# Kernel tuning notes

Hardware: AMD Instinct MI355X
Metric: run time of the kernel (lower is better)

Reference implementation:

```python
import jax, jax.numpy as jnp
import numpy as np


def _gcn_conv(x, edge_index, edge_weight, W, b, n_nodes):
    # PyG GCNConv with normalize=True: add self-loops (weight 1), symmetric norm,
    # transform then aggregate: out[col] += norm * (x @ W)[row], plus bias.
    row = jnp.concatenate([edge_index[0], jnp.arange(n_nodes)])
    col = jnp.concatenate([edge_index[1], jnp.arange(n_nodes)])
    w = jnp.concatenate([edge_weight, jnp.ones((n_nodes,), x.dtype)])
    deg = jax.ops.segment_sum(w, col, num_segments=n_nodes)
    dinv = jnp.where(deg > 0, jax.lax.rsqrt(jnp.maximum(deg, 1e-12)), 0.0)
    norm = dinv[row] * w * dinv[col]            # [E+N]
    h = x @ W                                   # [N, out]
    msg = h[row] * norm[:, None]                # [E+N, out]
    out = jax.ops.segment_sum(msg, col, num_segments=n_nodes)
    return out + b


def setup_inputs() -> dict:
    key = jax.random.key(0)
    ks = jax.random.split(key, 6)
    N, E, F_IN, H, C = 50000, 800000, 512, 128, 40
    features = jax.random.normal(ks[0], (N, F_IN), jnp.float32)
    edge_index = jax.random.randint(ks[1], (2, E), 0, N, jnp.int64)
    edge_weight = jax.random.uniform(ks[2], (E,), jnp.float32)
    W1 = jax.random.normal(ks[3], (F_IN, H), jnp.float32) * 0.05
    b1 = jnp.zeros((H,), jnp.float32)
    W2 = jax.random.normal(ks[4], (H, C), jnp.float32) * 0.05
    b2 = jnp.zeros((C,), jnp.float32)
    return {"features": features, "edge_index": edge_index, "edge_weight": edge_weight,
            "W1": W1, "b1": b1, "W2": W2, "b2": b2}


def reference(features, edge_index, edge_weight, W1, b1, W2, b2):
    n_nodes = features.shape[0]
    x = _gcn_conv(features, edge_index, edge_weight, W1, b1, n_nodes)
    x = jax.nn.relu(x)
    # F.dropout(training=self.training): identity in eval mode
    x = _gcn_conv(x, edge_index, edge_weight, W2, b2, n_nodes)
    return jax.nn.log_softmax(x, axis=1)
```

## Files before the change

kernel.cpp:

```cpp
#include <hip/hip_runtime.h>
#include <math.h>

#define FIN  512
#define HDIM 128
#define CDIM 40
#define CPAD 48
#define CAP  64

typedef __attribute__((ext_vector_type(8))) short shortx8;
typedef __attribute__((ext_vector_type(4))) float f32x4;
typedef __attribute__((ext_vector_type(2))) float floatx2;

__device__ inline unsigned short f2bf(float x) {
    unsigned u = __builtin_bit_cast(unsigned, x);
    unsigned r = u + 0x7fffu + ((u >> 16) & 1u);
    return (unsigned short)(r >> 16);
}
__device__ inline float bfu(unsigned short v) { return __builtin_bit_cast(float, (unsigned)v << 16); }
__device__ inline float bflo(unsigned u) { return __builtin_bit_cast(float, u << 16); }
__device__ inline float bfhi(unsigned u) { return __builtin_bit_cast(float, u & 0xffff0000u); }
__device__ inline float wdec(unsigned p) { return __builtin_bit_cast(float, (p & 0x7fffu) << 16); }
__device__ inline unsigned char f2fp8(float x) {
    return (unsigned char)(__builtin_amdgcn_cvt_pk_fp8_f32(x, x, 0, false) & 0xff);
}
__device__ inline floatx2 fp8x2_dec(unsigned short v) {
    return __builtin_amdgcn_cvt_pk_f32_fp8((int)(unsigned)v, false);
}

__global__ void k_fill(const int* __restrict__ row, const int* __restrict__ col,
                       const float* __restrict__ w,
                       unsigned long long* __restrict__ cursor,
                       unsigned* __restrict__ bkt, int E) {
    int e = blockIdx.x * blockDim.x + threadIdx.x;
    if (e >= E) return;
    const int c = col[e];
    const float we = w[e];
    const unsigned long long wfix = (unsigned long long)(we * 4294967296.0f);
    const unsigned long long old = atomicAdd(&cursor[c], (1ULL << 40) | wfix);
    const int p = (int)(old >> 40);
    const unsigned wb = (__builtin_bit_cast(unsigned, we) + 0x8000u) >> 16;
    if (p < CAP) bkt[(size_t)c * CAP + p] = ((unsigned)row[e] << 15) | (wb & 0x7fffu);
}

#define PREPB 280
__global__ void k_prep(const float* __restrict__ W1, const float* __restrict__ W2,
                       unsigned short* __restrict__ W1T, unsigned short* __restrict__ W2T,
                       const unsigned long long* __restrict__ cursor,
                       int* __restrict__ cnt, float* __restrict__ dinv, int n) {
    const int b = blockIdx.x;
    if (b < PREPB) {
        const int i = b * 256 + threadIdx.x;
        if (i < FIN * HDIM) {
            const int k = i >> 7, nn = i & 127;
            W1T[nn * FIN + k] = f2bf(W1[i]);
        } else {
            const int j = i - FIN * HDIM;
            const int nn = j >> 7, k = j & 127;
            W2T[j] = (nn < CDIM) ? f2bf(W2[k * CDIM + nn]) : (unsigned short)0;
        }
    } else {
        const int i = (b - PREPB) * 256 + threadIdx.x;
        if (i < n) {
            const unsigned long long p = cursor[i];
            cnt[i] = min((int)(p >> 40), CAP);
            const float wsum = (float)(p & ((1ULL << 40) - 1)) * 2.3283064365386963e-10f;
            dinv[i] = rsqrtf(1.0f + wsum);
        }
    }
}

#define G1_LDA 72
__global__ __launch_bounds__(256) void k_gemm1(const float* __restrict__ A,
                                               const unsigned short* __restrict__ W1T,
                                               const float* __restrict__ dinv,
                                               unsigned char* __restrict__ h1f8, int M) {
    __shared__ short As[128 * G1_LDA];
    __shared__ short Bs[128 * G1_LDA];
    const int tid  = threadIdx.x;
    const int wave = tid >> 6;
    const int lane = tid & 63;
    const int quad = lane >> 4;
    const int mr   = lane & 15;
    const int m0w  = (wave & 1) * 64;
    const int n0w  = (wave >> 1) * 64;
    const int m0b  = blockIdx.x * 128;

    const int srow = tid >> 1;
    const int spart = tid & 1;

    f32x4 acc[4][4];
#pragma unroll
    for (int i = 0; i < 4; i++)
#pragma unroll
        for (int j = 0; j < 4; j++) acc[i][j] = (f32x4)0.f;

    const int grow = m0b + srow;
    const bool arow_ok = grow < M;
    const float* ap = A + (size_t)grow * FIN + spart * 32;
    const unsigned short* bp = W1T + (size_t)srow * FIN + spart * 32;

    for (int k0 = 0; k0 < FIN; k0 += 64) {
#pragma unroll
        for (int i = 0; i < 4; i++) {
            float4 v0 = make_float4(0.f, 0.f, 0.f, 0.f), v1 = v0;
            if (arow_ok) {
                v0 = *(const float4*)(ap + k0 + i * 8);
                v1 = *(const float4*)(ap + k0 + i * 8 + 4);
            }
            shortx8 pk;
            pk[0] = (short)f2bf(v0.x); pk[1] = (short)f2bf(v0.y);
            pk[2] = (short)f2bf(v0.z); pk[3] = (short)f2bf(v0.w);
            pk[4] = (short)f2bf(v1.x); pk[5] = (short)f2bf(v1.y);
            pk[6] = (short)f2bf(v1.z); pk[7] = (short)f2bf(v1.w);
            *(shortx8*)&As[srow * G1_LDA + spart * 32 + i * 8] = pk;
        }
#pragma unroll
        for (int i = 0; i < 4; i++)
            *(shortx8*)&Bs[srow * G1_LDA + spart * 32 + i * 8] =
                *(const shortx8*)(bp + k0 + i * 8);
        __syncthreads();

#pragma unroll
        for (int kk = 0; kk < 2; kk++) {
            shortx8 af[4], bfr[4];
#pragma unroll
            for (int mt = 0; mt < 4; mt++)
                af[mt] = *(shortx8*)&As[(m0w + mt * 16 + mr) * G1_LDA + kk * 32 + quad * 8];
#pragma unroll
            for (int nt = 0; nt < 4; nt++)
                bfr[nt] = *(shortx8*)&Bs[(n0w + nt * 16 + mr) * G1_LDA + kk * 32 + quad * 8];
#pragma unroll
            for (int mt = 0; mt < 4; mt++)
#pragma unroll
                for (int nt = 0; nt < 4; nt++)
                    acc[mt][nt] = __builtin_amdgcn_mfma_f32_16x16x32_bf16(
                        af[mt], bfr[nt], acc[mt][nt], 0, 0, 0);
        }
        __syncthreads();
    }
#pragma unroll
    for (int mt = 0; mt < 4; mt++)
#pragma unroll
        for (int r = 0; r < 4; r++) {
            const int om = m0b + m0w + mt * 16 + quad * 4 + r;
            if (om < M) {
                const float dv = dinv[om];
#pragma unroll
                for (int nt = 0; nt < 4; nt++)
                    h1f8[(size_t)om * HDIM + n0w + nt * 16 + mr] = f2fp8(dv * acc[mt][nt][r]);
            }
        }
}

__global__ __launch_bounds__(256) void k_gather1(
    const int* __restrict__ cnt_arr, const unsigned* __restrict__ bkt,
    const unsigned char* __restrict__ h1f8,
    const float* __restrict__ dinv, const float* __restrict__ b1,
    unsigned* __restrict__ x1u, int n_nodes) {
    const int node = blockIdx.x * 4 + (threadIdx.x >> 6);
    const int lane = threadIdx.x & 63;
    if (node >= n_nodes) return;
    const int cnt = cnt_arr[node];
    const unsigned* base = bkt + (size_t)node * CAP;
    const int loff = lane * 2;
    float a0 = 0.f, a1 = 0.f, c0 = 0.f, c1 = 0.f;
    int s = 0;
    for (; s + 8 <= cnt; s += 8) {
        const uint4 qa = *(const uint4*)(base + s);
        const uint4 qb = *(const uint4*)(base + s + 4);
        const unsigned short v0 = *(const unsigned short*)(h1f8 + (size_t)(qa.x >> 15) * HDIM + loff);
        const unsigned short v1 = *(const unsigned short*)(h1f8 + (size_t)(qa.y >> 15) * HDIM + loff);
        const unsigned short v2 = *(const unsigned short*)(h1f8 + (size_t)(qa.z >> 15) * HDIM + loff);
        const unsigned short v3 = *(const unsigned short*)(h1f8 + (size_t)(qa.w >> 15) * HDIM + loff);
        const unsigned short v4 = *(const unsigned short*)(h1f8 + (size_t)(qb.x >> 15) * HDIM + loff);
        const unsigned short v5 = *(const unsigned short*)(h1f8 + (size_t)(qb.y >> 15) * HDIM + loff);
        const unsigned short v6 = *(const unsigned short*)(h1f8 + (size_t)(qb.z >> 15) * HDIM + loff);
        const unsigned short v7 = *(const unsigned short*)(h1f8 + (size_t)(qb.w >> 15) * HDIM + loff);
        const floatx2 f0 = fp8x2_dec(v0), f1 = fp8x2_dec(v1), f2 = fp8x2_dec(v2), f3 = fp8x2_dec(v3);
        const floatx2 f4 = fp8x2_dec(v4), f5 = fp8x2_dec(v5), f6 = fp8x2_dec(v6), f7 = fp8x2_dec(v7);
        a0 += wdec(qa.x) * f0.x + wdec(qa.y) * f1.x + wdec(qa.z) * f2.x + wdec(qa.w) * f3.x;
        a1 += wdec(qa.x) * f0.y + wdec(qa.y) * f1.y + wdec(qa.z) * f2.y + wdec(qa.w) * f3.y;
        c0 += wdec(qb.x) * f4.x + wdec(qb.y) * f5.x + wdec(qb.z) * f6.x + wdec(qb.w) * f7.x;
        c1 += wdec(qb.x) * f4.y + wdec(qb.y) * f5.y + wdec(qb.z) * f6.y + wdec(qb.w) * f7.y;
    }
    for (; s + 4 <= cnt; s += 4) {
        const uint4 qa = *(const uint4*)(base + s);
        const unsigned short v0 = *(const unsigned short*)(h1f8 + (size_t)(qa.x >> 15) * HDIM + loff);
        const unsigned short v1 = *(const unsigned short*)(h1f8 + (size_t)(qa.y >> 15) * HDIM + loff);
        const unsigned short v2 = *(const unsigned short*)(h1f8 + (size_t)(qa.z >> 15) * HDIM + loff);
        const unsigned short v3 = *(const unsigned short*)(h1f8 + (size_t)(qa.w >> 15) * HDIM + loff);
        const floatx2 f0 = fp8x2_dec(v0), f1 = fp8x2_dec(v1), f2 = fp8x2_dec(v2), f3 = fp8x2_dec(v3);
        a0 += wdec(qa.x) * f0.x + wdec(qa.y) * f1.x + wdec(qa.z) * f2.x + wdec(qa.w) * f3.x;
        a1 += wdec(qa.x) * f0.y + wdec(qa.y) * f1.y + wdec(qa.z) * f2.y + wdec(qa.w) * f3.y;
    }
    for (; s < cnt; s++) {
        const unsigned p = base[s];
        const unsigned short v = *(const unsigned short*)(h1f8 + (size_t)(p >> 15) * HDIM + loff);
        const floatx2 f = fp8x2_dec(v);
        a0 += wdec(p) * f.x;
        a1 += wdec(p) * f.y;
    }
    a0 += c0; a1 += c1;
    const float dl = dinv[node];
    const unsigned short vs = *(const unsigned short*)(h1f8 + (size_t)node * HDIM + loff);
    const floatx2 fs = fp8x2_dec(vs);
    a0 = fmaxf(dl * (a0 + fs.x) + b1[loff], 0.f);
    a1 = fmaxf(dl * (a1 + fs.y) + b1[loff + 1], 0.f);
    x1u[(size_t)node * 64 + lane] = (unsigned)f2bf(a0) | ((unsigned)f2bf(a1) << 16);
}

#define G2_LDA 136
__global__ __launch_bounds__(256) void k_gemm2(const unsigned short* __restrict__ x1bf,
                                               const unsigned short* __restrict__ W2T,
                                               const float* __restrict__ dinv,
                                               unsigned short* __restrict__ h2a,
                                               unsigned short* __restrict__ h2b, int M) {
    __shared__ short Xs[128 * G2_LDA];
    __shared__ short Ws[CPAD * G2_LDA];
    const int tid  = threadIdx.x;
    const int wave = tid >> 6;
    const int lane = tid & 63;
    const int quad = lane >> 4;
    const int mr   = lane & 15;
    const int m0b  = blockIdx.x * 128;

    {
        const int srow = tid >> 1, spart = tid & 1;
        const int grow = m0b + srow;
        if (grow < M) {
            const unsigned short* xp = x1bf + (size_t)grow * HDIM + spart * 64;
#pragma unroll
            for (int i = 0; i < 8; i++)
                *(shortx8*)&Xs[srow * G2_LDA + spart * 64 + i * 8] = *(const shortx8*)(xp + i * 8);
        } else {
#pragma unroll
            for (int i = 0; i < 8; i++)
                *(shortx8*)&Xs[srow * G2_LDA + spart * 64 + i * 8] = (shortx8)0;
        }
        for (int idx = tid; idx < CPAD * 16; idx += 256) {
            const int r = idx >> 4, j = idx & 15;
            *(shortx8*)&Ws[r * G2_LDA + j * 8] = *(const shortx8*)(W2T + r * HDIM + j * 8);
        }
    }
    __syncthreads();

    f32x4 acc[2][3];
#pragma unroll
    for (int i = 0; i < 2; i++)
#pragma unroll
        for (int j = 0; j < 3; j++) acc[i][j] = (f32x4)0.f;

    const int m0w = wave * 32;
#pragma unroll
    for (int kk = 0; kk < 4; kk++) {
        shortx8 af[2], bfr[3];
#pragma unroll
        for (int mt = 0; mt < 2; mt++)
            af[mt] = *(shortx8*)&Xs[(m0w + mt * 16 + mr) * G2_LDA + kk * 32 + quad * 8];
#pragma unroll
        for (int nt = 0; nt < 3; nt++)
            bfr[nt] = *(shortx8*)&Ws[(nt * 16 + mr) * G2_LDA + kk * 32 + quad * 8];
#pragma unroll
        for (int mt = 0; mt < 2; mt++)
#pragma unroll
            for (int nt = 0; nt < 3; nt++)
                acc[mt][nt] = __builtin_amdgcn_mfma_f32_16x16x32_bf16(
                    af[mt], bfr[nt], acc[mt][nt], 0, 0, 0);
    }
#pragma unroll
    for (int mt = 0; mt < 2; mt++)
#pragma unroll
        for (int r = 0; r < 4; r++) {
            const int om = m0b + m0w + mt * 16 + quad * 4 + r;
            if (om < M) {
                const float dv = dinv[om];
#pragma unroll
                for (int nt = 0; nt < 2; nt++)
                    h2a[(size_t)om * 32 + nt * 16 + mr] = f2bf(dv * acc[mt][nt][r]);
                if (mr < 8)
                    h2b[(size_t)om * 8 + mr] = f2bf(dv * acc[mt][2][r]);
            }
        }
}

__global__ __launch_bounds__(256) void k_gather2(
    const int* __restrict__ cnt_arr, const unsigned* __restrict__ bkt,
    const unsigned short* __restrict__ h2a, const unsigned short* __restrict__ h2b,
    const float* __restrict__ dinv, const float* __restrict__ b2,
    float* __restrict__ out, int n_nodes) {
    const int node = blockIdx.x * 4 + (threadIdx.x >> 6);
    const int lane = threadIdx.x & 63;
    if (node >= n_nodes) return;
    const bool act = lane < CDIM;
    const int cnt = cnt_arr[node];
    const unsigned* base = bkt + (size_t)node * CAP;
    const unsigned short* hb = (lane < 32) ? (h2a + lane) : (h2b + (lane & 31 & 7));
    const int hstride = (lane < 32) ? 32 : 8;
    float acc = 0.f, accb = 0.f;
    int s = 0;
    for (; s + 4 <= cnt; s += 4) {
        const uint4 q = *(const uint4*)(base + s);
        if (act) {
            acc  += wdec(q.x) * bfu(hb[(size_t)(q.x >> 15) * hstride])
                  + wdec(q.y) * bfu(hb[(size_t)(q.y >> 15) * hstride]);
            accb += wdec(q.z) * bfu(hb[(size_t)(q.z >> 15) * hstride])
                  + wdec(q.w) * bfu(hb[(size_t)(q.w >> 15) * hstride]);
        }
    }
    for (; s < cnt; s++) {
        const unsigned p = base[s];
        if (act) acc += wdec(p) * bfu(hb[(size_t)(p >> 15) * hstride]);
    }
    acc += accb;
    if (act) {
        const float dl = dinv[node];
        acc = dl * (acc + bfu(hb[(size_t)node * hstride])) + b2[lane];
    }
    float m = act ? acc : -INFINITY;
#pragma unroll
    for (int off = 32; off; off >>= 1) m = fmaxf(m, __shfl_xor(m, off));
    float se = act ? expf(acc - m) : 0.f;
#pragma unroll
    for (int off = 32; off; off >>= 1) se += __shfl_xor(se, off);
    if (act) out[(size_t)node * CDIM + lane] = acc - m - logf(se);
}

extern "C" void kernel_launch(void* const* d_in, const int* in_sizes, int n_in,
                              void* d_out, int out_size, void* d_ws, size_t ws_size,
                              hipStream_t stream) {
    const float* features = (const float*)d_in[0];
    const int*   eidx     = (const int*)d_in[1];
    const float* ew       = (const float*)d_in[2];
    const float* W1       = (const float*)d_in[3];
    const float* b1       = (const float*)d_in[4];
    const float* W2       = (const float*)d_in[5];
    const float* b2       = (const float*)d_in[6];
    float* out = (float*)d_out;

    const int Nn = in_sizes[0] / FIN;
    const int E  = in_sizes[2];
    const int* row = eidx;
    const int* col = eidx + E;

    char* ws = (char*)d_ws;
    size_t off = 0;
    auto alloc = [&](size_t bytes) { void* p = ws + off; off += (bytes + 255) & ~(size_t)255; return p; };
    unsigned long long* cursor = (unsigned long long*)alloc((size_t)Nn * 8);
    int*      cnt          = (int*)     alloc((size_t)Nn * 4);
    float*    dinv         = (float*)   alloc((size_t)Nn * 4);
    unsigned* bkt          = (unsigned*)alloc((size_t)Nn * CAP * 4);
    unsigned short* W1T    = (unsigned short*)alloc((size_t)FIN * HDIM * 2);
    unsigned short* W2T    = (unsigned short*)alloc((size_t)CPAD * HDIM * 2);
    unsigned char*  h1f8   = (unsigned char*) alloc((size_t)Nn * HDIM);
    unsigned short* x1bf   = (unsigned short*)alloc((size_t)Nn * HDIM * 2);
    unsigned short* h2a    = (unsigned short*)alloc((size_t)Nn * 32 * 2);
    unsigned short* h2b    = (unsigned short*)alloc((size_t)Nn * 8 * 2);

    hipMemsetAsync(cursor, 0, (size_t)Nn * 8, stream);
    k_fill<<<(E + 255) / 256, 256, 0, stream>>>(row, col, ew, cursor, bkt, E);
    k_prep<<<PREPB + (Nn + 255) / 256, 256, 0, stream>>>(W1, W2, W1T, W2T,
                                                         cursor, cnt, dinv, Nn);
    k_gemm1<<<(Nn + 127) / 128, 256, 0, stream>>>(features, W1T, dinv, h1f8, Nn);
    k_gather1<<<(Nn + 3) / 4, 256, 0, stream>>>(cnt, bkt, h1f8, dinv, b1,
                                                (unsigned*)x1bf, Nn);
    k_gemm2<<<(Nn + 127) / 128, 256, 0, stream>>>(x1bf, W2T, dinv, h2a, h2b, Nn);
    k_gather2<<<(Nn + 3) / 4, 256, 0, stream>>>(cnt, bkt, h2a, h2b, dinv, b2, out, Nn);
}
```

Measured before the change: 304.4 us.

## Fuse layer-1 gather with layer-2 GEMM and shrink GEMM1 tile to 64 rows

Merges the first aggregation kernel and the second small GEMM into one kernel. Each block gathers 64 nodes' aggregated rows into shared memory as bf16 and then multiplies them by W2 with MFMA, so the x1 intermediate never round-trips through global memory. The weight transposes move into the edge-fill kernel as extra blocks. GEMM1 uses 64-row tiles to roughly double the block count. The cost is that each gather wave now processes 16 nodes serially, which lowers memory-level parallelism in the gather, and W2T fragments are read straight from global memory.

```diff
diff --git a/kernel.cpp b/kernel.cpp
--- a/kernel.cpp
+++ b/kernel.cpp
@@ -17,8 +17,6 @@
     return (unsigned short)(r >> 16);
 }
 __device__ inline float bfu(unsigned short v) { return __builtin_bit_cast(float, (unsigned)v << 16); }
-__device__ inline float bflo(unsigned u) { return __builtin_bit_cast(float, u << 16); }
-__device__ inline float bfhi(unsigned u) { return __builtin_bit_cast(float, u & 0xffff0000u); }
 __device__ inline float wdec(unsigned p) { return __builtin_bit_cast(float, (p & 0x7fffu) << 16); }
 __device__ inline unsigned char f2fp8(float x) {
     return (unsigned char)(__builtin_amdgcn_cvt_pk_fp8_f32(x, x, 0, false) & 0xff);
@@ -27,11 +25,26 @@
     return __builtin_amdgcn_cvt_pk_f32_fp8((int)(unsigned)v, false);
 }
 
+#define PREPB 280
 __global__ void k_fill(const int* __restrict__ row, const int* __restrict__ col,
                        const float* __restrict__ w,
                        unsigned long long* __restrict__ cursor,
-                       unsigned* __restrict__ bkt, int E) {
-    int e = blockIdx.x * blockDim.x + threadIdx.x;
+                       unsigned* __restrict__ bkt, int E, int eblocks,
+                       const float* __restrict__ W1, const float* __restrict__ W2,
+                       unsigned short* __restrict__ W1T, unsigned short* __restrict__ W2T) {
+    if ((int)blockIdx.x >= eblocks) {
+        const int i = ((int)blockIdx.x - eblocks) * 256 + (int)threadIdx.x;
+        if (i < FIN * HDIM) {
+            const int k = i >> 7, nn = i & 127;
+            W1T[nn * FIN + k] = f2bf(W1[i]);
+        } else {
+            const int j = i - FIN * HDIM;
+            const int nn = j >> 7, k = j & 127;
+            W2T[j] = (nn < CDIM) ? f2bf(W2[k * CDIM + nn]) : (unsigned short)0;
+        }
+        return;
+    }
+    const int e = blockIdx.x * blockDim.x + threadIdx.x;
     if (e >= E) return;
     const int c = col[e];
     const float we = w[e];
@@ -42,30 +55,14 @@
     if (p < CAP) bkt[(size_t)c * CAP + p] = ((unsigned)row[e] << 15) | (wb & 0x7fffu);
 }
 
-#define PREPB 280
-__global__ void k_prep(const float* __restrict__ W1, const float* __restrict__ W2,
-                       unsigned short* __restrict__ W1T, unsigned short* __restrict__ W2T,
-                       const unsigned long long* __restrict__ cursor,
+__global__ void k_prep(const unsigned long long* __restrict__ cursor,
                        int* __restrict__ cnt, float* __restrict__ dinv, int n) {
-    const int b = blockIdx.x;
-    if (b < PREPB) {
-        const int i = b * 256 + threadIdx.x;
-        if (i < FIN * HDIM) {
-            const int k = i >> 7, nn = i & 127;
-            W1T[nn * FIN + k] = f2bf(W1[i]);
-        } else {
-            const int j = i - FIN * HDIM;
-            const int nn = j >> 7, k = j & 127;
-            W2T[j] = (nn < CDIM) ? f2bf(W2[k * CDIM + nn]) : (unsigned short)0;
-        }
-    } else {
-        const int i = (b - PREPB) * 256 + threadIdx.x;
-        if (i < n) {
-            const unsigned long long p = cursor[i];
-            cnt[i] = min((int)(p >> 40), CAP);
-            const float wsum = (float)(p & ((1ULL << 40) - 1)) * 2.3283064365386963e-10f;
-            dinv[i] = rsqrtf(1.0f + wsum);
-        }
+    const int i = blockIdx.x * 256 + threadIdx.x;
+    if (i < n) {
+        const unsigned long long p = cursor[i];
+        cnt[i] = min((int)(p >> 40), CAP);
+        const float wsum = (float)(p & ((1ULL << 40) - 1)) * 2.3283064365386963e-10f;
+        dinv[i] = rsqrtf(1.0f + wsum);
     }
 }
 
@@ -74,36 +71,35 @@
                                                const unsigned short* __restrict__ W1T,
                                                const float* __restrict__ dinv,
                                                unsigned char* __restrict__ h1f8, int M) {
-    __shared__ short As[128 * G1_LDA];
+    __shared__ short As[64 * G1_LDA];
     __shared__ short Bs[128 * G1_LDA];
     const int tid  = threadIdx.x;
     const int wave = tid >> 6;
     const int lane = tid & 63;
     const int quad = lane >> 4;
     const int mr   = lane & 15;
-    const int m0w  = (wave & 1) * 64;
-    const int n0w  = (wave >> 1) * 64;
-    const int m0b  = blockIdx.x * 128;
-
-    const int srow = tid >> 1;
-    const int spart = tid & 1;
-
-    f32x4 acc[4][4];
+    const int n0w  = wave * 32;
+    const int m0b  = blockIdx.x * 64;
+
+    const int srowA = tid >> 2, spartA = tid & 3;
+    const int srowB = tid >> 1, spartB = tid & 1;
+
+    f32x4 acc[4][2];
 #pragma unroll
     for (int i = 0; i < 4; i++)
 #pragma unroll
-        for (int j = 0; j < 4; j++) acc[i][j] = (f32x4)0.f;
-
-    const int grow = m0b + srow;
-    const bool arow_ok = grow < M;
-    const float* ap = A + (size_t)grow * FIN + spart * 32;
-    const unsigned short* bp = W1T + (size_t)srow * FIN + spart * 32;
+        for (int j = 0; j < 2; j++) acc[i][j] = (f32x4)0.f;
+
+    const int growA = m0b + srowA;
+    const bool okA = growA < M;
+    const float* ap = A + (size_t)growA * FIN + spartA * 16;
+    const unsigned short* bp = W1T + (size_t)srowB * FIN + spartB * 32;
 
     for (int k0 = 0; k0 < FIN; k0 += 64) {
 #pragma unroll
-        for (int i = 0; i < 4; i++) {
+        for (int i = 0; i < 2; i++) {
             float4 v0 = make_float4(0.f, 0.f, 0.f, 0.f), v1 = v0;
-            if (arow_ok) {
+            if (okA) {
                 v0 = *(const float4*)(ap + k0 + i * 8);
                 v1 = *(const float4*)(ap + k0 + i * 8 + 4);
             }
@@ -112,27 +108,27 @@
             pk[2] = (short)f2bf(v0.z); pk[3] = (short)f2bf(v0.w);
             pk[4] = (short)f2bf(v1.x); pk[5] = (short)f2bf(v1.y);
             pk[6] = (short)f2bf(v1.z); pk[7] = (short)f2bf(v1.w);
-            *(shortx8*)&As[srow * G1_LDA + spart * 32 + i * 8] = pk;
+            *(shortx8*)&As[srowA * G1_LDA + spartA * 16 + i * 8] = pk;
         }
 #pragma unroll
         for (int i = 0; i < 4; i++)
-            *(shortx8*)&Bs[srow * G1_LDA + spart * 32 + i * 8] =
+            *(shortx8*)&Bs[srowB * G1_LDA + spartB * 32 + i * 8] =
                 *(const shortx8*)(bp + k0 + i * 8);
         __syncthreads();
 
 #pragma unroll
         for (int kk = 0; kk < 2; kk++) {
-            shortx8 af[4], bfr[4];
+            shortx8 af[4], bfr[2];
 #pragma unroll
             for (int mt = 0; mt < 4; mt++)
-                af[mt] = *(shortx8*)&As[(m0w + mt * 16 + mr) * G1_LDA + kk * 32 + quad * 8];
-#pragma unroll
-            for (int nt = 0; nt < 4; nt++)
+                af[mt] = *(shortx8*)&As[(mt * 16 + mr) * G1_LDA + kk * 32 + quad * 8];
+#pragma unroll
+            for (int nt = 0; nt < 2; nt++)
                 bfr[nt] = *(shortx8*)&Bs[(n0w + nt * 16 + mr) * G1_LDA + kk * 32 + quad * 8];
 #pragma unroll
             for (int mt = 0; mt < 4; mt++)
 #pragma unroll
-                for (int nt = 0; nt < 4; nt++)
+                for (int nt = 0; nt < 2; nt++)
                     acc[mt][nt] = __builtin_amdgcn_mfma_f32_16x16x32_bf16(
                         af[mt], bfr[nt], acc[mt][nt], 0, 0, 0);
         }
@@ -142,145 +138,113 @@
     for (int mt = 0; mt < 4; mt++)
 #pragma unroll
         for (int r = 0; r < 4; r++) {
-            const int om = m0b + m0w + mt * 16 + quad * 4 + r;
+            const int om = m0b + mt * 16 + quad * 4 + r;
             if (om < M) {
                 const float dv = dinv[om];
 #pragma unroll
-                for (int nt = 0; nt < 4; nt++)
+                for (int nt = 0; nt < 2; nt++)
                     h1f8[(size_t)om * HDIM + n0w + nt * 16 + mr] = f2fp8(dv * acc[mt][nt][r]);
             }
         }
 }
 
-__global__ __launch_bounds__(256) void k_gather1(
+#define G2_LDA 136
+__global__ __launch_bounds__(256) void k_g1g2(
     const int* __restrict__ cnt_arr, const unsigned* __restrict__ bkt,
     const unsigned char* __restrict__ h1f8,
     const float* __restrict__ dinv, const float* __restrict__ b1,
-    unsigned* __restrict__ x1u, int n_nodes) {
-    const int node = blockIdx.x * 4 + (threadIdx.x >> 6);
-    const int lane = threadIdx.x & 63;
-    if (node >= n_nodes) return;
-    const int cnt = cnt_arr[node];
-    const unsigned* base = bkt + (size_t)node * CAP;
-    const int loff = lane * 2;
-    float a0 = 0.f, a1 = 0.f, c0 = 0.f, c1 = 0.f;
-    int s = 0;
-    for (; s + 8 <= cnt; s += 8) {
-        const uint4 qa = *(const uint4*)(base + s);
-        const uint4 qb = *(const uint4*)(base + s + 4);
-        const unsigned short v0 = *(const unsigned short*)(h1f8 + (size_t)(qa.x >> 15) * HDIM + loff);
-        const unsigned short v1 = *(const unsigned short*)(h1f8 + (size_t)(qa.y >> 15) * HDIM + loff);
-        const unsigned short v2 = *(const unsigned short*)(h1f8 + (size_t)(qa.z >> 15) * HDIM + loff);
-        const unsigned short v3 = *(const unsigned short*)(h1f8 + (size_t)(qa.w >> 15) * HDIM + loff);
-        const unsigned short v4 = *(const unsigned short*)(h1f8 + (size_t)(qb.x >> 15) * HDIM + loff);
-        const unsigned short v5 = *(const unsigned short*)(h1f8 + (size_t)(qb.y >> 15) * HDIM + loff);
-        const unsigned short v6 = *(const unsigned short*)(h1f8 + (size_t)(qb.z >> 15) * HDIM + loff);
-        const unsigned short v7 = *(const unsigned short*)(h1f8 + (size_t)(qb.w >> 15) * HDIM + loff);
-        const floatx2 f0 = fp8x2_dec(v0), f1 = fp8x2_dec(v1), f2 = fp8x2_dec(v2), f3 = fp8x2_dec(v3);
-        const floatx2 f4 = fp8x2_dec(v4), f5 = fp8x2_dec(v5), f6 = fp8x2_dec(v6), f7 = fp8x2_dec(v7);
-        a0 += wdec(qa.x) * f0.x + wdec(qa.y) * f1.x + wdec(qa.z) * f2.x + wdec(qa.w) * f3.x;
-        a1 += wdec(qa.x) * f0.y + wdec(qa.y) * f1.y + wdec(qa.z) * f2.y + wdec(qa.w) * f3.y;
-        c0 += wdec(qb.x) * f4.x + wdec(qb.y) * f5.x + wdec(qb.z) * f6.x + wdec(qb.w) * f7.x;
-        c1 += wdec(qb.x) * f4.y + wdec(qb.y) * f5.y + wdec(qb.z) * f6.y + wdec(qb.w) * f7.y;
-    }
-    for (; s + 4 <= cnt; s += 4) {
-        const uint4 qa = *(const uint4*)(base + s);
-        const unsigned short v0 = *(const unsigned short*)(h1f8 + (size_t)(qa.x >> 15) * HDIM + loff);
-        const unsigned short v1 = *(const unsigned short*)(h1f8 + (size_t)(qa.y >> 15) * HDIM + loff);
-        const unsigned short v2 = *(const unsigned short*)(h1f8 + (size_t)(qa.z >> 15) * HDIM + loff);
-        const unsigned short v3 = *(const unsigned short*)(h1f8 + (size_t)(qa.w >> 15) * HDIM + loff);
-        const floatx2 f0 = fp8x2_dec(v0), f1 = fp8x2_dec(v1), f2 = fp8x2_dec(v2), f3 = fp8x2_dec(v3);
-        a0 += wdec(qa.x) * f0.x + wdec(qa.y) * f1.x + wdec(qa.z) * f2.x + wdec(qa.w) * f3.x;
-        a1 += wdec(qa.x) * f0.y + wdec(qa.y) * f1.y + wdec(qa.z) * f2.y + wdec(qa.w) * f3.y;
-    }
-    for (; s < cnt; s++) {
-        const unsigned p = base[s];
-        const unsigned short v = *(const unsigned short*)(h1f8 + (size_t)(p >> 15) * HDIM + loff);
-        const floatx2 f = fp8x2_dec(v);
-        a0 += wdec(p) * f.x;
-        a1 += wdec(p) * f.y;
-    }
-    a0 += c0; a1 += c1;
-    const float dl = dinv[node];
-    const unsigned short vs = *(const unsigned short*)(h1f8 + (size_t)node * HDIM + loff);
-    const floatx2 fs = fp8x2_dec(vs);
-    a0 = fmaxf(dl * (a0 + fs.x) + b1[loff], 0.f);
-    a1 = fmaxf(dl * (a1 + fs.y) + b1[loff + 1], 0.f);
-    x1u[(size_t)node * 64 + lane] = (unsigned)f2bf(a0) | ((unsigned)f2bf(a1) << 16);
-}
-
-#define G2_LDA 136
-__global__ __launch_bounds__(256) void k_gemm2(const unsigned short* __restrict__ x1bf,
-                                               const unsigned short* __restrict__ W2T,
-                                               const float* __restrict__ dinv,
-                                               unsigned short* __restrict__ h2a,
-                                               unsigned short* __restrict__ h2b, int M) {
-    __shared__ short Xs[128 * G2_LDA];
-    __shared__ short Ws[CPAD * G2_LDA];
+    const unsigned short* __restrict__ W2T,
+    unsigned short* __restrict__ h2a, unsigned short* __restrict__ h2b,
+    int n_nodes) {
+    __shared__ short Xs[64 * G2_LDA];
     const int tid  = threadIdx.x;
     const int wave = tid >> 6;
     const int lane = tid & 63;
+    const int loff = lane * 2;
+    const int m0b  = blockIdx.x * 64;
+    const float bias0 = b1[loff], bias1 = b1[loff + 1];
+
+    for (int i = 0; i < 16; i++) {
+        const int node = m0b + wave * 16 + i;
+        unsigned val = 0u;
+        if (node < n_nodes) {
+            const int cnt = cnt_arr[node];
+            const unsigned* base = bkt + (size_t)node * CAP;
+            float a0 = 0.f, a1 = 0.f, c0 = 0.f, c1 = 0.f;
+            int s = 0;
+            for (; s + 8 <= cnt; s += 8) {
+                const uint4 qa = *(const uint4*)(base + s);
+                const uint4 qb = *(const uint4*)(base + s + 4);
+                const unsigned short v0 = *(const unsigned short*)(h1f8 + (size_t)(qa.x >> 15) * HDIM + loff);
+                const unsigned short v1 = *(const unsigned short*)(h1f8 + (size_t)(qa.y >> 15) * HDIM + loff);
+                const unsigned short v2 = *(const unsigned short*)(h1f8 + (size_t)(qa.z >> 15) * HDIM + loff);
+                const unsigned short v3 = *(const unsigned short*)(h1f8 + (size_t)(qa.w >> 15) * HDIM + loff);
+                const unsigned short v4 = *(const unsigned short*)(h1f8 + (size_t)(qb.x >> 15) * HDIM + loff);
+                const unsigned short v5 = *(const unsigned short*)(h1f8 + (size_t)(qb.y >> 15) * HDIM + loff);
+                const unsigned short v6 = *(const unsigned short*)(h1f8 + (size_t)(qb.z >> 15) * HDIM + loff);
+                const unsigned short v7 = *(const unsigned short*)(h1f8 + (size_t)(qb.w >> 15) * HDIM + loff);
+                const floatx2 f0 = fp8x2_dec(v0), f1 = fp8x2_dec(v1), f2 = fp8x2_dec(v2), f3 = fp8x2_dec(v3);
+                const floatx2 f4 = fp8x2_dec(v4), f5 = fp8x2_dec(v5), f6 = fp8x2_dec(v6), f7 = fp8x2_dec(v7);
+                a0 += wdec(qa.x) * f0.x + wdec(qa.y) * f1.x + wdec(qa.z) * f2.x + wdec(qa.w) * f3.x;
+                a1 += wdec(qa.x) * f0.y + wdec(qa.y) * f1.y + wdec(qa.z) * f2.y + wdec(qa.w) * f3.y;
+                c0 += wdec(qb.x) * f4.x + wdec(qb.y) * f5.x + wdec(qb.z) * f6.x + wdec(qb.w) * f7.x;
+                c1 += wdec(qb.x) * f4.y + wdec(qb.y) * f5.y + wdec(qb.z) * f6.y + wdec(qb.w) * f7.y;
+            }
+            for (; s + 4 <= cnt; s += 4) {
+                const uint4 qa = *(const uint4*)(base + s);
+                const unsigned short v0 = *(const unsigned short*)(h1f8 + (size_t)(qa.x >> 15) * HDIM + loff);
+                const unsigned short v1 = *(const unsigned short*)(h1f8 + (size_t)(qa.y >> 15) * HDIM + loff);
+                const unsigned short v2 = *(const unsigned short*)(h1f8 + (size_t)(qa.z >> 15) * HDIM + loff);
+                const unsigned short v3 = *(const unsigned short*)(h1f8 + (size_t)(qa.w >> 15) * HDIM + loff);
+                const floatx2 f0 = fp8x2_dec(v0), f1 = fp8x2_dec(v1), f2 = fp8x2_dec(v2), f3 = fp8x2_dec(v3);
+                a0 += wdec(qa.x) * f0.x + wdec(qa.y) * f1.x + wdec(qa.z) * f2.x + wdec(qa.w) * f3.x;
+                a1 += wdec(qa.x) * f0.y + wdec(qa.y) * f1.y + wdec(qa.z) * f2.y + wdec(qa.w) * f3.y;
+            }
+            for (; s < cnt; s++) {
+                const unsigned p = base[s];
+                const unsigned short v = *(const unsigned short*)(h1f8 + (size_t)(p >> 15) * HDIM + loff);
+                const floatx2 f = fp8x2_dec(v);
+                a0 += wdec(p) * f.x;
+                a1 += wdec(p) * f.y;
+            }
+            a0 += c0; a1 += c1;
+            const float dl = dinv[node];
+            const unsigned short vs = *(const unsigned short*)(h1f8 + (size_t)node * HDIM + loff);
+            const floatx2 fs = fp8x2_dec(vs);
+            a0 = fmaxf(dl * (a0 + fs.x) + bias0, 0.f);
+            a1 = fmaxf(dl * (a1 + fs.y) + bias1, 0.f);
+            val = (unsigned)f2bf(a0) | ((unsigned)f2bf(a1) << 16);
+        }
+        *(unsigned*)&Xs[(wave * 16 + i) * G2_LDA + loff] = val;
+    }
+    __syncthreads();
+
     const int quad = lane >> 4;
     const int mr   = lane & 15;
-    const int m0b  = blockIdx.x * 128;
-
-    {
-        const int srow = tid >> 1, spart = tid & 1;
-        const int grow = m0b + srow;
-        if (grow < M) {
-            const unsigned short* xp = x1bf + (size_t)grow * HDIM + spart * 64;
-#pragma unroll
-            for (int i = 0; i < 8; i++)
-                *(shortx8*)&Xs[srow * G2_LDA + spart * 64 + i * 8] = *(const shortx8*)(xp + i * 8);
-        } else {
-#pragma unroll
-            for (int i = 0; i < 8; i++)
-                *(shortx8*)&Xs[srow * G2_LDA + spart * 64 + i * 8] = (shortx8)0;
-        }
-        for (int idx = tid; idx < CPAD * 16; idx += 256) {
-            const int r = idx >> 4, j = idx & 15;
-            *(shortx8*)&Ws[r * G2_LDA + j * 8] = *(const shortx8*)(W2T + r * HDIM + j * 8);
-        }
-    }
-    __syncthreads();
-
-    f32x4 acc[2][3];
-#pragma unroll
-    for (int i = 0; i < 2; i++)
-#pragma unroll
-        for (int j = 0; j < 3; j++) acc[i][j] = (f32x4)0.f;
-
-    const int m0w = wave * 32;
+    f32x4 acc[3];
+#pragma unroll
+    for (int nt = 0; nt < 3; nt++) acc[nt] = (f32x4)0.f;
 #pragma unroll
     for (int kk = 0; kk < 4; kk++) {
-        shortx8 af[2], bfr[3];
-#pragma unroll
-        for (int mt = 0; mt < 2; mt++)
-            af[mt] = *(shortx8*)&Xs[(m0w + mt * 16 + mr) * G2_LDA + kk * 32 + quad * 8];
-#pragma unroll
-        for (int nt = 0; nt < 3; nt++)
-            bfr[nt] = *(shortx8*)&Ws[(nt * 16 + mr) * G2_LDA + kk * 32 + quad * 8];
-#pragma unroll
-        for (int mt = 0; mt < 2; mt++)
-#pragma unroll
-            for (int nt = 0; nt < 3; nt++)
-                acc[mt][nt] = __builtin_amdgcn_mfma_f32_16x16x32_bf16(
-                    af[mt], bfr[nt], acc[mt][nt], 0, 0, 0);
-    }
-#pragma unroll
-    for (int mt = 0; mt < 2; mt++)
-#pragma unroll
-        for (int r = 0; r < 4; r++) {
-            const int om = m0b + m0w + mt * 16 + quad * 4 + r;
-            if (om < M) {
-                const float dv = dinv[om];
-#pragma unroll
-                for (int nt = 0; nt < 2; nt++)
-                    h2a[(size_t)om * 32 + nt * 16 + mr] = f2bf(dv * acc[mt][nt][r]);
-                if (mr < 8)
-                    h2b[(size_t)om * 8 + mr] = f2bf(dv * acc[mt][2][r]);
-            }
-        }
+        const shortx8 af = *(const shortx8*)&Xs[(wave * 16 + mr) * G2_LDA + kk * 32 + quad * 8];
+#pragma unroll
+        for (int nt = 0; nt < 3; nt++) {
+            const shortx8 bfr = *(const shortx8*)(W2T + (size_t)(nt * 16 + mr) * HDIM + kk * 32 + quad * 8);
+            acc[nt] = __builtin_amdgcn_mfma_f32_16x16x32_bf16(af, bfr, acc[nt], 0, 0, 0);
+        }
+    }
+#pragma unroll
+    for (int r = 0; r < 4; r++) {
+        const int om = m0b + wave * 16 + quad * 4 + r;
+        if (om < n_nodes) {
+            const float dv = dinv[om];
+#pragma unroll
+            for (int nt = 0; nt < 2; nt++)
+                h2a[(size_t)om * 32 + nt * 16 + mr] = f2bf(dv * acc[nt][r]);
+            if (mr < 8)
+                h2b[(size_t)om * 8 + mr] = f2bf(dv * acc[2][r]);
+        }
+    }
 }
 
 __global__ __launch_bounds__(256) void k_gather2(
@@ -352,17 +316,17 @@
     unsigned short* W1T    = (unsigned short*)alloc((size_t)FIN * HDIM * 2);
     unsigned short* W2T    = (unsigned short*)alloc((size_t)CPAD * HDIM * 2);
     unsigned char*  h1f8   = (unsigned char*) alloc((size_t)Nn * HDIM);
-    unsigned short* x1bf   = (unsigned short*)alloc((size_t)Nn * HDIM * 2);
     unsigned short* h2a    = (unsigned short*)alloc((size_t)Nn * 32 * 2);
     unsigned short* h2b    = (unsigned short*)alloc((size_t)Nn * 8 * 2);
 
+    const int eblocks = (E + 255) / 256;
+
     hipMemsetAsync(cursor, 0, (size_t)Nn * 8, stream);
-    k_fill<<<(E + 255) / 256, 256, 0, stream>>>(row, col, ew, cursor, bkt, E);
-    k_prep<<<PREPB + (Nn + 255) / 256, 256, 0, stream>>>(W1, W2, W1T, W2T,
-                                                         cursor, cnt, dinv, Nn);
-    k_gemm1<<<(Nn + 127) / 128, 256, 0, stream>>>(features, W1T, dinv, h1f8, Nn);
-    k_gather1<<<(Nn + 3) / 4, 256, 0, stream>>>(cnt, bkt, h1f8, dinv, b1,
-                                                (unsigned*)x1bf, Nn);
-    k_gemm2<<<(Nn + 127) / 128, 256, 0, stream>>>(x1bf, W2T, dinv, h2a, h2b, Nn);
+    k_fill<<<eblocks + PREPB, 256, 0, stream>>>(row, col, ew, cursor, bkt, E, eblocks,
+                                                W1, W2, W1T, W2T);
+    k_prep<<<(Nn + 255) / 256, 256, 0, stream>>>(cursor, cnt, dinv, Nn);
+    k_gemm1<<<(Nn + 63) / 64, 256, 0, stream>>>(features, W1T, dinv, h1f8, Nn);
+    k_g1g2<<<(Nn + 63) / 64, 256, 0, stream>>>(cnt, bkt, h1f8, dinv, b1, W2T,
+                                               h2a, h2b, Nn);
     k_gather2<<<(Nn + 3) / 4, 256, 0, stream>>>(cnt, bkt, h2a, h2b, dinv, b2, out, Nn);
 }
```

New measurement: 333.7 us. 9.6% more time.
